# Performance work log

Measured on AMD Instinct MI355X. Metric: run time of the kernel, lower is better.

## Reference

```python
import jax, jax.numpy as jnp
import numpy as np

N, E, R = 50000, 300000, 4
F_IN, H, G, T = 11, 256, 2048, 19
BN_EPS = 1e-5


def _init_lin(key, fan_in, fan_out, extra=()):
    k1, k2 = jax.random.split(key)
    s = 1.0 / np.sqrt(fan_in)
    W = jax.random.uniform(k1, extra + (fan_in, fan_out), jnp.float32, -s, s)
    b = jax.random.uniform(k2, extra + (fan_out,), jnp.float32, -s, s)
    return W, b


def setup_inputs() -> dict:
    key = jax.random.key(0)
    ks = jax.random.split(key, 32)
    inp = {
        "x": jax.random.normal(ks[0], (N, F_IN), jnp.float32),
        "edge_index": jax.random.randint(ks[1], (2, E), 0, N, jnp.int64),
        "edge_type": jax.random.randint(ks[2], (E,), 0, R, jnp.int64),
        "batch": jnp.sort(jax.random.randint(ks[3], (N,), 0, G, jnp.int64)),
    }
    ki = 4
    for li, fin in ((1, F_IN), (2, H), (3, H)):
        sw, sb = _init_lin(ks[ki], fin, H); ki += 1
        w1, b1 = _init_lin(ks[ki], fin, H, (R,)); ki += 1
        w2, b2 = _init_lin(ks[ki], H, H, (R,)); ki += 1
        inp[f"l{li}_sw"], inp[f"l{li}_sb"] = sw, sb
        inp[f"l{li}_w1"], inp[f"l{li}_b1"] = w1, b1
        inp[f"l{li}_g"] = jnp.ones((R, H), jnp.float32)
        inp[f"l{li}_bt"] = jnp.zeros((R, H), jnp.float32)
        inp[f"l{li}_w2"], inp[f"l{li}_b2"] = w2, b2
    inp["lin_w"], inp["lin_b"] = _init_lin(ks[ki], H, T)
    return inp


def _rgin_layer(x, src, dst, rel_mask, sw, sb, w1, b1, g, bt, w2, b2):
    # self-loop linear
    out = x @ sw + sb
    msg = x[src]  # [E, d] gather of source features
    for i in range(R):
        # per-relation masked scatter-add aggregation at target nodes
        agg = jax.ops.segment_sum(msg * rel_mask[:, i:i + 1], dst, num_segments=N)
        h = x + agg  # GIN with eps=0: (1+eps)*x + sum_neighbors
        h = h @ w1[i] + b1[i]
        # BatchNorm1d (training-mode batch stats, biased var)
        mu = jnp.mean(h, axis=0)
        var = jnp.var(h, axis=0)
        h = (h - mu) * jax.lax.rsqrt(var + BN_EPS) * g[i] + bt[i]
        h = jax.nn.relu(h)
        out = out + h @ w2[i] + b2[i]
    return out


def reference(x, edge_index, edge_type, batch,
              l1_sw, l1_sb, l1_w1, l1_b1, l1_g, l1_bt, l1_w2, l1_b2,
              l2_sw, l2_sb, l2_w1, l2_b1, l2_g, l2_bt, l2_w2, l2_b2,
              l3_sw, l3_sb, l3_w1, l3_b1, l3_g, l3_bt, l3_w2, l3_b2,
              lin_w, lin_b):
    src, dst = edge_index[0], edge_index[1]
    rel_mask = jax.nn.one_hot(edge_type, R, dtype=x.dtype)  # [E, R]
    h = jax.nn.relu(_rgin_layer(x, src, dst, rel_mask, l1_sw, l1_sb, l1_w1, l1_b1, l1_g, l1_bt, l1_w2, l1_b2))
    h = jax.nn.relu(_rgin_layer(h, src, dst, rel_mask, l2_sw, l2_sb, l2_w1, l2_b1, l2_g, l2_bt, l2_w2, l2_b2))
    h = jax.nn.relu(_rgin_layer(h, src, dst, rel_mask, l3_sw, l3_sb, l3_w1, l3_b1, l3_g, l3_bt, l3_w2, l3_b2))
    # global mean pool over graphs
    pooled = jax.ops.segment_sum(h, batch, num_segments=G)
    counts = jax.ops.segment_sum(jnp.ones((N,), h.dtype), batch, num_segments=G)
    pooled = pooled / jnp.maximum(counts, 1.0)[:, None]
    return pooled @ lin_w + lin_b
```

## Files before the change

### kernel.cpp

```cpp
#include <hip/hip_runtime.h>

static const int kN = 50000;
static const int kE = 300000;
static const int kG = 2048;
static const int kT = 19;
static const int kSeg = kN * 4;
static const int kScanB = (kSeg + 256) / 256;

typedef __bf16 bf16;
typedef __bf16 bf16x8 __attribute__((ext_vector_type(8)));
typedef __bf16 bf16x4 __attribute__((ext_vector_type(4)));
typedef float  f32x4  __attribute__((ext_vector_type(4)));

__global__ __launch_bounds__(512) void k_rgin1(
    const bf16* __restrict__ Pb, const int* __restrict__ srcidx,
    const int* __restrict__ row_ptr, const bf16* __restrict__ w1t,
    bf16* __restrict__ h1, float* __restrict__ stats)
{
    __shared__ bf16 As[64][264];
    const int t = threadIdx.x;
    const int r = blockIdx.y;
    const int m0 = blockIdx.x * 64;
    const int wave = t >> 6, lane = t & 63;
    const int l15 = lane & 15, lq = lane >> 4, koff = lq * 8;
    const int wn = wave * 32;

    const bf16* Bt = w1t + (long)r * 65536;
    const bf16* Bp[2];
#pragma unroll
    for (int j = 0; j < 2; ++j)
        Bp[j] = Bt + (long)(wn + j * 16 + l15) * 256 + koff;
    bf16x8 b0[2], b1[2];
#pragma unroll
    for (int j = 0; j < 2; ++j) b0[j] = *(const bf16x8*)(Bp[j]);

    {
        const int rbase = m0 + wave * 8;
        int i0s[8], i1s[8];
#pragma unroll
        for (int rr = 0; rr < 8; ++rr) {
            int dc = rbase + rr; if (dc >= kN) dc = kN - 1;
            int seg = dc * 4 + r;
            i0s[rr] = row_ptr[seg];
            i1s[rr] = row_ptr[seg + 1];
        }
#pragma unroll
        for (int rr = 0; rr < 8; ++rr) {
            int dc = rbase + rr; if (dc >= kN) dc = kN - 1;
            bf16x4 sv = ((const bf16x4*)(Pb + (long)dc * 256))[lane];
            f32x4 a = {(float)sv[0], (float)sv[1], (float)sv[2], (float)sv[3]};
            int i = i0s[rr], i1 = i1s[rr];
            for (; i + 1 < i1; i += 2) {
                int s0 = srcidx[i], s1 = srcidx[i + 1];
                bf16x4 v0 = ((const bf16x4*)(Pb + (long)s0 * 256))[lane];
                bf16x4 v1 = ((const bf16x4*)(Pb + (long)s1 * 256))[lane];
                a[0] += (float)v0[0] + (float)v1[0];
                a[1] += (float)v0[1] + (float)v1[1];
                a[2] += (float)v0[2] + (float)v1[2];
                a[3] += (float)v0[3] + (float)v1[3];
            }
            if (i < i1) {
                bf16x4 v0 = ((const bf16x4*)(Pb + (long)srcidx[i] * 256))[lane];
                a[0] += (float)v0[0]; a[1] += (float)v0[1];
                a[2] += (float)v0[2]; a[3] += (float)v0[3];
            }
            bf16x4 o = {(bf16)a[0], (bf16)a[1], (bf16)a[2], (bf16)a[3]};
            *(bf16x4*)&As[wave * 8 + rr][lane * 4] = o;
        }
    }
    __syncthreads();

    const bf16* Ar[4];
#pragma unroll
    for (int i = 0; i < 4; ++i) Ar[i] = &As[i * 16 + l15][koff];

    f32x4 acc[4][2];
#pragma unroll
    for (int i = 0; i < 4; ++i)
#pragma unroll
        for (int j = 0; j < 2; ++j) acc[i][j] = (f32x4){0.f, 0.f, 0.f, 0.f};

#pragma unroll
    for (int kt = 0; kt < 256; kt += 32) {
        int kn = kt + 32; if (kn >= 256) kn = 0;
#pragma unroll
        for (int j = 0; j < 2; ++j) b1[j] = *(const bf16x8*)(Bp[j] + kn);
        bf16x8 a[4];
#pragma unroll
        for (int i = 0; i < 4; ++i) a[i] = *(const bf16x8*)(Ar[i] + kt);
#pragma unroll
        for (int i = 0; i < 4; ++i)
#pragma unroll
            for (int j = 0; j < 2; ++j)
                acc[i][j] = __builtin_amdgcn_mfma_f32_16x16x32_bf16(a[i], b0[j], acc[i][j], 0, 0, 0);
#pragma unroll
        for (int j = 0; j < 2; ++j) b0[j] = b1[j];
    }

    const int cB = r * 256;
    float sv[2] = {0, 0}, qv[2] = {0, 0};
#pragma unroll
    for (int i = 0; i < 4; ++i) {
        int rowb = m0 + i * 16 + lq * 4;
#pragma unroll
        for (int rr = 0; rr < 4; ++rr) {
            int gm = rowb + rr;
            if (gm < kN) {
#pragma unroll
                for (int j = 0; j < 2; ++j) {
                    int gn = wn + j * 16 + l15;
                    bf16 bv = (bf16)acc[i][j][rr];
                    h1[(long)gm * 1024 + cB + gn] = bv;
                    float f = (float)bv;
                    sv[j] += f; qv[j] += f * f;
                }
            }
        }
    }
#pragma unroll
    for (int j = 0; j < 2; ++j) {
        float s = sv[j], q = qv[j];
        s += __shfl_xor(s, 16); s += __shfl_xor(s, 32);
        q += __shfl_xor(q, 16); q += __shfl_xor(q, 32);
        if (lq == 0) {
            int gn = cB + wn + j * 16 + l15;
            atomicAdd(&stats[gn], s);
            atomicAdd(&stats[1024 + gn], q);
        }
    }
}

__global__ __launch_bounds__(512) void k_l1gemm(
    const bf16* __restrict__ a1b, const bf16* __restrict__ w1tL1,
    bf16* __restrict__ h1, float* __restrict__ stats)
{
    const int t = threadIdx.x;
    const int r = blockIdx.y;
    const int m0 = blockIdx.x * 128;
    const int wave = t >> 6, lane = t & 63;
    const int l15 = lane & 15, lq = lane >> 4, koff = lq * 8;
    const int wm = (wave & 1) * 64, wn = (wave >> 1) * 64;

    bf16x8 a[4], b[4];
#pragma unroll
    for (int i = 0; i < 4; ++i) {
        int gm = m0 + wm + i * 16 + l15;
        if (gm >= kN) gm = kN - 1;
        a[i] = *(const bf16x8*)(a1b + ((long)r * kN + gm) * 32 + koff);
    }
#pragma unroll
    for (int j = 0; j < 4; ++j)
        b[j] = *(const bf16x8*)(w1tL1 + (long)r * 8192 + (long)(wn + j * 16 + l15) * 32 + koff);

    f32x4 acc[4][4];
#pragma unroll
    for (int i = 0; i < 4; ++i)
#pragma unroll
        for (int j = 0; j < 4; ++j)
            acc[i][j] = __builtin_amdgcn_mfma_f32_16x16x32_bf16(a[i], b[j],
                        (f32x4){0.f, 0.f, 0.f, 0.f}, 0, 0, 0);

    const int cB = r * 256;
    float sv[4] = {0,0,0,0}, qv[4] = {0,0,0,0};
#pragma unroll
    for (int i = 0; i < 4; ++i) {
        int rowb = m0 + wm + i * 16 + lq * 4;
#pragma unroll
        for (int rr = 0; rr < 4; ++rr) {
            int gm = rowb + rr;
            if (gm < kN) {
#pragma unroll
                for (int j = 0; j < 4; ++j) {
                    int gn = wn + j * 16 + l15;
                    bf16 bv = (bf16)acc[i][j][rr];
                    h1[(long)gm * 1024 + cB + gn] = bv;
                    float f = (float)bv;
                    sv[j] += f; qv[j] += f * f;
                }
            }
        }
    }
#pragma unroll
    for (int j = 0; j < 4; ++j) {
        float s = sv[j], q = qv[j];
        s += __shfl_xor(s, 16); s += __shfl_xor(s, 32);
        q += __shfl_xor(q, 16); q += __shfl_xor(q, 32);
        if (lq == 0) {
            int gn = cB + wn + j * 16 + l15;
            atomicAdd(&stats[gn], s);
            atomicAdd(&stats[1024 + gn], q);
        }
    }
}

template<int CHUNKS, int C1, bool PoolOut>
__global__ __launch_bounds__(256) void k_gemm2(
    const bf16* __restrict__ A1, int lda1,
    const bf16* __restrict__ A2,
    const bf16* __restrict__ Bt,
    bf16* __restrict__ Cout,
    int M, const float* __restrict__ bias,
    const float* __restrict__ scl, const float* __restrict__ shf,
    const int* __restrict__ batch, float* __restrict__ pooled)
{
    constexpr int K = CHUNKS * 128;
    __shared__ bf16 As[2][64][136];
    const int t = threadIdx.x;
    const int wave = t >> 6, lane = t & 63;
    const int l15 = lane & 15, lq = lane >> 4, koff = lq * 8;
    const int wn = wave * 64;
    const int m0 = blockIdx.x * 64;

    const int srow = t >> 4;
    const int kg   = (t & 15) * 8;

    const bf16* Bp[4];
#pragma unroll
    for (int j = 0; j < 4; ++j)
        Bp[j] = Bt + (long)(wn + j * 16 + l15) * K + koff;

    f32x4 acc[4][4];
#pragma unroll
    for (int i = 0; i < 4; ++i)
#pragma unroll
        for (int j = 0; j < 4; ++j) acc[i][j] = (f32x4){0.f, 0.f, 0.f, 0.f};

    auto ld_raw = [&](int c, bf16x8* rv, float4* sf) {
#pragma unroll
        for (int i = 0; i < 4; ++i) {
            int gm = m0 + srow + i * 16; if (gm >= M) gm = M - 1;
            if (c < C1) rv[i] = *(const bf16x8*)(A1 + (long)gm * lda1 + c * 128 + kg);
            else        rv[i] = *(const bf16x8*)(A2 + (long)gm * 1024 + (c - C1) * 128 + kg);
        }
        if (c >= C1) {
            int k2 = (c - C1) * 128 + kg;
            sf[0] = *(const float4*)(scl + k2);
            sf[1] = *(const float4*)(scl + k2 + 4);
            sf[2] = *(const float4*)(shf + k2);
            sf[3] = *(const float4*)(shf + k2 + 4);
        }
    };
    auto st_lds = [&](int c, const bf16x8* rv, const float4* sf, int sel) {
        float sa[8], ta[8];
        if (c >= C1) {
            sa[0]=sf[0].x; sa[1]=sf[0].y; sa[2]=sf[0].z; sa[3]=sf[0].w;
            sa[4]=sf[1].x; sa[5]=sf[1].y; sa[6]=sf[1].z; sa[7]=sf[1].w;
            ta[0]=sf[2].x; ta[1]=sf[2].y; ta[2]=sf[2].z; ta[3]=sf[2].w;
            ta[4]=sf[3].x; ta[5]=sf[3].y; ta[6]=sf[3].z; ta[7]=sf[3].w;
        }
#pragma unroll
        for (int i = 0; i < 4; ++i) {
            bf16x8 v = rv[i];
            if (c >= C1) {
                bf16x8 o;
#pragma unroll
                for (int u = 0; u < 8; ++u)
                    o[u] = (bf16)fmaxf(0.f, fmaf((float)v[u], sa[u], ta[u]));
                v = o;
            }
            *(bf16x8*)&As[sel][srow + i * 16][kg] = v;
        }
    };

    bf16x8 rv[4]; float4 sf[4];
    ld_raw(0, rv, sf);
    bf16x8 breg[2][4];
#pragma unroll
    for (int j = 0; j < 4; ++j) breg[0][j] = *(const bf16x8*)(Bp[j]);
#pragma unroll
    for (int j = 0; j < 4; ++j) breg[1][j] = *(const bf16x8*)(Bp[j] + 32);
    st_lds(0, rv, sf, 0);
    __syncthreads();

    for (int c = 0; c < CHUNKS; ++c) {
        const int sel = c & 1;
        if (c + 1 < CHUNKS) ld_raw(c + 1, rv, sf);
#pragma unroll
        for (int ks = 0; ks < 4; ++ks) {
            bf16x8 a[4], bu[4];
#pragma unroll
            for (int i = 0; i < 4; ++i)
                a[i] = *(const bf16x8*)&As[sel][i * 16 + l15][ks * 32 + koff];
#pragma unroll
            for (int j = 0; j < 4; ++j) bu[j] = breg[ks & 1][j];
            int knext = (c * 4 + ks + 2) * 32; if (knext >= K) knext = 0;
#pragma unroll
            for (int j = 0; j < 4; ++j) breg[ks & 1][j] = *(const bf16x8*)(Bp[j] + knext);
#pragma unroll
            for (int i = 0; i < 4; ++i)
#pragma unroll
                for (int j = 0; j < 4; ++j)
                    acc[i][j] = __builtin_amdgcn_mfma_f32_16x16x32_bf16(a[i], bu[j], acc[i][j], 0, 0, 0);
        }
        if (c + 1 < CHUNKS) {
            st_lds(c + 1, rv, sf, sel ^ 1);
            __syncthreads();
        }
    }

#pragma unroll
    for (int i = 0; i < 4; ++i) {
        int rowb = m0 + i * 16 + lq * 4;
#pragma unroll
        for (int rr = 0; rr < 4; ++rr) {
            int gm = rowb + rr;
            if (gm < M) {
                int g = PoolOut ? batch[gm] : 0;
#pragma unroll
                for (int j = 0; j < 4; ++j) {
                    int gn = wn + j * 16 + l15;
                    float v = fmaxf(acc[i][j][rr] + bias[gn], 0.f);
                    if (PoolOut) atomicAdd(&pooled[(long)g * 256 + gn], v);
                    else         Cout[(long)gm * 256 + gn] = (bf16)v;
                }
            }
        }
    }
}

__global__ void k_hist(const int* __restrict__ ei, const int* __restrict__ et,
                       int* __restrict__ hist)
{
    int e = blockIdx.x * 256 + threadIdx.x;
    if (e >= kE) return;
    atomicAdd(&hist[ei[kE + e] * 4 + et[e]], 1);
}

__global__ void k_scan1(const int* __restrict__ hist, int* __restrict__ bsum)
{
    __shared__ int sd[256];
    int i = blockIdx.x * 256 + threadIdx.x;
    sd[threadIdx.x] = (i < kSeg) ? hist[i] : 0;
    __syncthreads();
    for (int o = 128; o > 0; o >>= 1) {
        if (threadIdx.x < o) sd[threadIdx.x] += sd[threadIdx.x + o];
        __syncthreads();
    }
    if (threadIdx.x == 0) bsum[blockIdx.x] = sd[0];
}

__global__ __launch_bounds__(1024) void k_scan2(const int* __restrict__ bsum,
                                                int* __restrict__ boff)
{
    __shared__ int sd[1024];
    int t = threadIdx.x;
    sd[t] = (t < kScanB) ? bsum[t] : 0;
    __syncthreads();
    for (int o = 1; o < 1024; o <<= 1) {
        int v = (t >= o) ? sd[t - o] : 0;
        __syncthreads();
        sd[t] += v;
        __syncthreads();
    }
    if (t < kScanB) boff[t] = (t == 0) ? 0 : sd[t - 1];
}

__global__ void k_scan3(const int* __restrict__ hist, const int* __restrict__ boff,
                        int* __restrict__ row_ptr, int* __restrict__ cursor)
{
    __shared__ int sd[256];
    int i = blockIdx.x * 256 + threadIdx.x;
    int v = (i < kSeg) ? hist[i] : 0;
    sd[threadIdx.x] = v;
    __syncthreads();
    for (int o = 1; o < 256; o <<= 1) {
        int u = (threadIdx.x >= o) ? sd[threadIdx.x - o] : 0;
        __syncthreads();
        sd[threadIdx.x] += u;
        __syncthreads();
    }
    if (i <= kSeg) {
        int excl = boff[blockIdx.x] + sd[threadIdx.x] - v;
        row_ptr[i] = excl;
        if (i < kSeg) cursor[i] = excl;
    }
}

__global__ void k_fill(const int* __restrict__ ei, const int* __restrict__ et,
                       int* __restrict__ cursor, int* __restrict__ srcidx)
{
    int e = blockIdx.x * 256 + threadIdx.x;
    if (e >= kE) return;
    int key = ei[kE + e] * 4 + et[e];
    int pos = atomicAdd(&cursor[key], 1);
    srcidx[pos] = ei[e];
}

__global__ void k_agg11(const float* __restrict__ x, const int* __restrict__ srcidx,
                        const int* __restrict__ row_ptr, bf16* __restrict__ a1b)
{
    long gid = (long)blockIdx.x * 256 + threadIdx.x;
    if (gid >= (long)kSeg * 32) return;
    int ch  = (int)(gid & 31);
    int seg = (int)(gid >> 5);
    int d = seg >> 2, r = seg & 3;
    float acc = 0.f;
    if (ch < 11) {
        acc = x[(long)d * 11 + ch];
        int i0 = row_ptr[seg], i1 = row_ptr[seg + 1];
        for (int i = i0; i < i1; ++i) acc += x[(long)srcidx[i] * 11 + ch];
    }
    a1b[((long)r * kN + d) * 32 + ch] = (bf16)acc;
}

__global__ void k_xpad(const float* __restrict__ x, bf16* __restrict__ xb1)
{
    long gid = (long)blockIdx.x * 256 + threadIdx.x;
    if (gid >= (long)kN * 128) return;
    int c = (int)(gid & 127); long d = gid >> 7;
    xb1[gid] = (c < 11) ? (bf16)x[d * 11 + c] : (bf16)0.f;
}

__global__ void k_wt_s(const float* __restrict__ in, bf16* __restrict__ out,
                       int K, int N, int ldout, int coff)
{
    int i = blockIdx.x * 256 + threadIdx.x;
    if (i >= K * N) return;
    int n = i / K, k = i - n * K;
    out[(long)n * ldout + coff + k] = (bf16)in[(long)k * N + n];
}

__global__ void k_wtL1(const float* __restrict__ w1, bf16* __restrict__ out)
{
    int i = blockIdx.x * 256 + threadIdx.x;
    if (i >= 4 * 256 * 32) return;
    int r = i >> 13, rem = i & 8191, n = rem >> 5, k = rem & 31;
    out[i] = (k < 11) ? (bf16)w1[(long)r * 11 * 256 + (long)k * 256 + n] : (bf16)0.f;
}

__global__ void k_bn_params(const float* __restrict__ stats,
                            const float* __restrict__ g, const float* __restrict__ bt,
                            float* __restrict__ scl, float* __restrict__ shf)
{
    int c = blockIdx.x * 256 + threadIdx.x;
    const float invN = 1.0f / (float)kN;
    float mu  = stats[c] * invN;
    float var = stats[1024 + c] * invN - mu * mu;
    float sc  = g[c] * rsqrtf(var + 1e-5f);
    scl[c] = sc;
    shf[c] = bt[c] - mu * sc;
}

__global__ void k_bias_total(const float* sb0, const float* b20,
                             const float* sb1, const float* b21,
                             const float* sb2, const float* b22,
                             float* __restrict__ btt)
{
    int l = blockIdx.x, j = threadIdx.x;
    const float* sb = (l == 0) ? sb0 : (l == 1) ? sb1 : sb2;
    const float* b2 = (l == 0) ? b20 : (l == 1) ? b21 : b22;
    float v = sb[j];
#pragma unroll
    for (int r = 0; r < 4; ++r) v += b2[r * 256 + j];
    btt[l * 256 + j] = v;
}

__global__ void k_counts(const int* __restrict__ batch, float* __restrict__ counts)
{
    int v = blockIdx.x * 256 + threadIdx.x;
    if (v < kN) atomicAdd(&counts[batch[v]], 1.0f);
}

__global__ __launch_bounds__(64) void k_head(const float* __restrict__ pooled,
                                             const float* __restrict__ counts,
                                             const float* __restrict__ lw,
                                             const float* __restrict__ lb,
                                             float* __restrict__ out)
{
    int g = blockIdx.x;
    int l = threadIdx.x;
    float inv = 1.0f / fmaxf(counts[g], 1.0f);
    float acc[kT];
#pragma unroll
    for (int t = 0; t < kT; ++t) acc[t] = 0.f;
    for (int k = l; k < 256; k += 64) {
        float p = pooled[((long)g << 8) + k] * inv;
#pragma unroll
        for (int t = 0; t < kT; ++t) acc[t] = fmaf(p, lw[k * kT + t], acc[t]);
    }
#pragma unroll
    for (int off = 32; off > 0; off >>= 1)
#pragma unroll
        for (int t = 0; t < kT; ++t) acc[t] += __shfl_down(acc[t], off);
    if (l == 0) {
#pragma unroll
        for (int t = 0; t < kT; ++t) out[(long)g * kT + t] = acc[t] + lb[t];
    }
}

extern "C" void kernel_launch(void* const* d_in, const int* in_sizes, int n_in,
                              void* d_out, int out_size, void* d_ws, size_t ws_size,
                              hipStream_t stream)
{
    const float* x     = (const float*)d_in[0];
    const int*   ei    = (const int*)d_in[1];
    const int*   et    = (const int*)d_in[2];
    const int*   batch = (const int*)d_in[3];

    const float *sw[3], *sb[3], *w1[3], *gmm[3], *btm[3], *w2[3], *b2[3];
    for (int l = 0; l < 3; ++l) {
        int b = 4 + l * 8;
        sw[l]  = (const float*)d_in[b + 0];
        sb[l]  = (const float*)d_in[b + 1];
        w1[l]  = (const float*)d_in[b + 2];
        gmm[l] = (const float*)d_in[b + 4];
        btm[l] = (const float*)d_in[b + 5];
        w2[l]  = (const float*)d_in[b + 6];
        b2[l]  = (const float*)d_in[b + 7];
    }
    const float* lin_w = (const float*)d_in[28];
    const float* lin_b = (const float*)d_in[29];
    float* out = (float*)d_out;
    (void)in_sizes; (void)n_in; (void)out_size;

    char* wsb = (char*)d_ws;
    size_t off = 0;
    auto alloc = [&](size_t bytes) { void* p = wsb + off; off = (off + bytes + 255) & ~(size_t)255; return p; };
    bf16*  Pb0    = (bf16*) alloc((size_t)kN * 256 * 2);
    bf16*  Pb1    = (bf16*) alloc((size_t)kN * 256 * 2);
    bf16*  h1     = (bf16*) alloc((size_t)kN * 1024 * 2);
    bf16*  a1b    = (bf16*) alloc((size_t)4 * kN * 32 * 2);
    bf16*  xb1    = (bf16*) alloc((size_t)kN * 128 * 2);
    bf16*  w1t    = (bf16*) alloc((size_t)2 * 4 * 65536 * 2);
    bf16*  w1tL1  = (bf16*) alloc((size_t)4 * 256 * 32 * 2);
    bf16*  Bc0    = (bf16*) alloc((size_t)256 * 1152 * 2);
    bf16*  Bc1    = (bf16*) alloc((size_t)256 * 1280 * 2);
    bf16*  Bc2    = (bf16*) alloc((size_t)256 * 1280 * 2);
    int*   hist   = (int*)  alloc((size_t)(kSeg + 1) * 4);
    int*   row_ptr= (int*)  alloc((size_t)(kSeg + 1) * 4);
    int*   cursor = (int*)  alloc((size_t)kSeg * 4);
    int*   srcidx = (int*)  alloc((size_t)kE * 4);
    int*   bsum   = (int*)  alloc((size_t)kScanB * 4);
    int*   boff   = (int*)  alloc((size_t)kScanB * 4);
    float* stats  = (float*)alloc(2048 * 4);
    float* scl    = (float*)alloc(1024 * 4);
    float* shf    = (float*)alloc(1024 * 4);
    float* btt    = (float*)alloc(3 * 256 * 4);
    float* pooled = (float*)alloc((size_t)kG * 256 * 4);
    float* counts = (float*)alloc(kG * 4);
    if (ws_size < off) return;

    const dim3 gL1((kN + 127) / 128, 4);
    const dim3 gR((kN + 63) / 64, 4);
    const dim3 g2((kN + 63) / 64);

    hipMemsetAsync(hist, 0, (size_t)(kSeg + 1) * 4, stream);
    k_hist<<<(kE + 255) / 256, 256, 0, stream>>>(ei, et, hist);
    k_scan1<<<kScanB, 256, 0, stream>>>(hist, bsum);
    k_scan2<<<1, 1024, 0, stream>>>(bsum, boff);
    k_scan3<<<kScanB, 256, 0, stream>>>(hist, boff, row_ptr, cursor);
    k_fill<<<(kE + 255) / 256, 256, 0, stream>>>(ei, et, cursor, srcidx);

    k_bias_total<<<3, 256, 0, stream>>>(sb[0], b2[0], sb[1], b2[1], sb[2], b2[2], btt);
    k_xpad<<<(int)(((long)kN * 128 + 255) / 256), 256, 0, stream>>>(x, xb1);
    k_wtL1<<<(4 * 256 * 32 + 255) / 256, 256, 0, stream>>>(w1[0], w1tL1);
    for (int l = 1; l < 3; ++l)
        for (int r = 0; r < 4; ++r)
            k_wt_s<<<256, 256, 0, stream>>>(w1[l] + (long)r * 65536,
                                            w1t + (long)(l - 1) * 4 * 65536 + (long)r * 65536,
                                            256, 256, 256, 0);
    hipMemsetAsync(Bc0, 0, (size_t)256 * 1152 * 2, stream);
    k_wt_s<<<(11 * 256 + 255) / 256, 256, 0, stream>>>(sw[0], Bc0, 11, 256, 1152, 0);
    k_wt_s<<<1024, 256, 0, stream>>>(w2[0], Bc0, 1024, 256, 1152, 128);
    k_wt_s<<<256, 256, 0, stream>>>(sw[1], Bc1, 256, 256, 1280, 0);
    k_wt_s<<<1024, 256, 0, stream>>>(w2[1], Bc1, 1024, 256, 1280, 256);
    k_wt_s<<<256, 256, 0, stream>>>(sw[2], Bc2, 256, 256, 1280, 0);
    k_wt_s<<<1024, 256, 0, stream>>>(w2[2], Bc2, 1024, 256, 1280, 256);

    k_counts<<<(kN + 255) / 256, 256, 0, stream>>>(batch, counts);
    hipMemsetAsync(pooled, 0, (size_t)kG * 256 * 4, stream);

    k_agg11<<<(int)(((long)kSeg * 32 + 255) / 256), 256, 0, stream>>>(x, srcidx, row_ptr, a1b);
    hipMemsetAsync(stats, 0, 2048 * 4, stream);
    k_l1gemm<<<gL1, 512, 0, stream>>>(a1b, w1tL1, h1, stats);
    k_bn_params<<<4, 256, 0, stream>>>(stats, gmm[0], btm[0], scl, shf);
    k_gemm2<9, 1, false><<<g2, 256, 0, stream>>>(xb1, 128, h1, Bc0,
                                                 Pb0, kN, btt + 0, scl, shf, nullptr, nullptr);

    hipMemsetAsync(stats, 0, 2048 * 4, stream);
    k_rgin1<<<gR, 512, 0, stream>>>(Pb0, srcidx, row_ptr, w1t, h1, stats);
    k_bn_params<<<4, 256, 0, stream>>>(stats, gmm[1], btm[1], scl, shf);
    k_gemm2<10, 2, false><<<g2, 256, 0, stream>>>(Pb0, 256, h1, Bc1,
                                                  Pb1, kN, btt + 256, scl, shf, nullptr, nullptr);

    hipMemsetAsync(stats, 0, 2048 * 4, stream);
    k_rgin1<<<gR, 512, 0, stream>>>(Pb1, srcidx, row_ptr, w1t + (size_t)4 * 65536, h1, stats);
    k_bn_params<<<4, 256, 0, stream>>>(stats, gmm[2], btm[2], scl, shf);
    k_gemm2<10, 2, true><<<g2, 256, 0, stream>>>(Pb1, 256, h1, Bc2,
                                                 nullptr, kN, btt + 512, scl, shf, batch, pooled);

    k_head<<<kG, 64, 0, stream>>>(pooled, counts, lin_w, lin_b, out);
}
```

Baseline: 1.004 ms.

## Restructure gemm2 to 512 threads with 2x4 wave tiling and 256-wide K chunks

The second-stage GEMM moves from 4 waves (each owning a 64x64 tile) to 8 waves arranged 2x4 (each owning a 32x64 tile). K is staged in 256-wide chunks with a single LDS buffer instead of double-buffered 128-wide chunks. Layer 1 is padded to K=1280 so all three layers share one code path, at the cost of a larger padded self-loop input and extra zero MACs. The aim is more waves per block to hide latency, but each B fragment now feeds only 2 MFMAs instead of 4, and the single buffer needs two barriers per chunk.

```diff
diff --git a/kernel.cpp b/kernel.cpp
--- a/kernel.cpp
+++ b/kernel.cpp
@@ -193,9 +193,9 @@
     }
 }
 
-template<int CHUNKS, int C1, bool PoolOut>
-__global__ __launch_bounds__(256) void k_gemm2(
-    const bf16* __restrict__ A1, int lda1,
+template<bool PoolOut>
+__global__ __launch_bounds__(512) void k_gemm2(
+    const bf16* __restrict__ A1,
     const bf16* __restrict__ A2,
     const bf16* __restrict__ Bt,
     bf16* __restrict__ Cout,
@@ -203,62 +203,63 @@
     const float* __restrict__ scl, const float* __restrict__ shf,
     const int* __restrict__ batch, float* __restrict__ pooled)
 {
-    constexpr int K = CHUNKS * 128;
-    __shared__ bf16 As[2][64][136];
+    constexpr int K = 1280;
+    __shared__ bf16 As[64][264];
     const int t = threadIdx.x;
     const int wave = t >> 6, lane = t & 63;
     const int l15 = lane & 15, lq = lane >> 4, koff = lq * 8;
-    const int wn = wave * 64;
+    const int wm = (wave & 1) * 32;
+    const int wn = (wave >> 1) * 64;
     const int m0 = blockIdx.x * 64;
 
-    const int srow = t >> 4;
-    const int kg   = (t & 15) * 8;
+    const int srow = t >> 5;
+    const int c8   = (t & 31) * 8;
 
     const bf16* Bp[4];
 #pragma unroll
     for (int j = 0; j < 4; ++j)
         Bp[j] = Bt + (long)(wn + j * 16 + l15) * K + koff;
 
-    f32x4 acc[4][4];
-#pragma unroll
-    for (int i = 0; i < 4; ++i)
+    f32x4 acc[2][4];
+#pragma unroll
+    for (int i = 0; i < 2; ++i)
 #pragma unroll
         for (int j = 0; j < 4; ++j) acc[i][j] = (f32x4){0.f, 0.f, 0.f, 0.f};
 
     auto ld_raw = [&](int c, bf16x8* rv, float4* sf) {
 #pragma unroll
-        for (int i = 0; i < 4; ++i) {
-            int gm = m0 + srow + i * 16; if (gm >= M) gm = M - 1;
-            if (c < C1) rv[i] = *(const bf16x8*)(A1 + (long)gm * lda1 + c * 128 + kg);
-            else        rv[i] = *(const bf16x8*)(A2 + (long)gm * 1024 + (c - C1) * 128 + kg);
-        }
-        if (c >= C1) {
-            int k2 = (c - C1) * 128 + kg;
+        for (int u = 0; u < 4; ++u) {
+            int gm = m0 + srow + u * 16; if (gm >= M) gm = M - 1;
+            if (c == 0) rv[u] = *(const bf16x8*)(A1 + (long)gm * 256 + c8);
+            else        rv[u] = *(const bf16x8*)(A2 + (long)gm * 1024 + (c - 1) * 256 + c8);
+        }
+        if (c > 0) {
+            int k2 = (c - 1) * 256 + c8;
             sf[0] = *(const float4*)(scl + k2);
             sf[1] = *(const float4*)(scl + k2 + 4);
             sf[2] = *(const float4*)(shf + k2);
             sf[3] = *(const float4*)(shf + k2 + 4);
         }
     };
-    auto st_lds = [&](int c, const bf16x8* rv, const float4* sf, int sel) {
+    auto st_lds = [&](int c, const bf16x8* rv, const float4* sf) {
         float sa[8], ta[8];
-        if (c >= C1) {
+        if (c > 0) {
             sa[0]=sf[0].x; sa[1]=sf[0].y; sa[2]=sf[0].z; sa[3]=sf[0].w;
             sa[4]=sf[1].x; sa[5]=sf[1].y; sa[6]=sf[1].z; sa[7]=sf[1].w;
             ta[0]=sf[2].x; ta[1]=sf[2].y; ta[2]=sf[2].z; ta[3]=sf[2].w;
             ta[4]=sf[3].x; ta[5]=sf[3].y; ta[6]=sf[3].z; ta[7]=sf[3].w;
         }
 #pragma unroll
-        for (int i = 0; i < 4; ++i) {
-            bf16x8 v = rv[i];
-            if (c >= C1) {
+        for (int u = 0; u < 4; ++u) {
+            bf16x8 v = rv[u];
+            if (c > 0) {
                 bf16x8 o;
 #pragma unroll
-                for (int u = 0; u < 8; ++u)
-                    o[u] = (bf16)fmaxf(0.f, fmaf((float)v[u], sa[u], ta[u]));
+                for (int w = 0; w < 8; ++w)
+                    o[w] = (bf16)fmaxf(0.f, fmaf((float)v[w], sa[w], ta[w]));
                 v = o;
             }
-            *(bf16x8*)&As[sel][srow + i * 16][kg] = v;
+            *(bf16x8*)&As[srow + u * 16][c8] = v;
         }
     };
 
@@ -269,38 +270,38 @@
     for (int j = 0; j < 4; ++j) breg[0][j] = *(const bf16x8*)(Bp[j]);
 #pragma unroll
     for (int j = 0; j < 4; ++j) breg[1][j] = *(const bf16x8*)(Bp[j] + 32);
-    st_lds(0, rv, sf, 0);
+    st_lds(0, rv, sf);
     __syncthreads();
 
-    for (int c = 0; c < CHUNKS; ++c) {
-        const int sel = c & 1;
-        if (c + 1 < CHUNKS) ld_raw(c + 1, rv, sf);
-#pragma unroll
-        for (int ks = 0; ks < 4; ++ks) {
-            bf16x8 a[4], bu[4];
-#pragma unroll
-            for (int i = 0; i < 4; ++i)
-                a[i] = *(const bf16x8*)&As[sel][i * 16 + l15][ks * 32 + koff];
+    for (int c = 0; c < 5; ++c) {
+        if (c + 1 < 5) ld_raw(c + 1, rv, sf);
+#pragma unroll
+        for (int ks = 0; ks < 8; ++ks) {
+            bf16x8 a[2], bu[4];
+#pragma unroll
+            for (int i = 0; i < 2; ++i)
+                a[i] = *(const bf16x8*)&As[wm + i * 16 + l15][ks * 32 + koff];
 #pragma unroll
             for (int j = 0; j < 4; ++j) bu[j] = breg[ks & 1][j];
-            int knext = (c * 4 + ks + 2) * 32; if (knext >= K) knext = 0;
+            int knext = c * 256 + (ks + 2) * 32; if (knext >= K) knext = 0;
 #pragma unroll
             for (int j = 0; j < 4; ++j) breg[ks & 1][j] = *(const bf16x8*)(Bp[j] + knext);
 #pragma unroll
-            for (int i = 0; i < 4; ++i)
+            for (int i = 0; i < 2; ++i)
 #pragma unroll
                 for (int j = 0; j < 4; ++j)
                     acc[i][j] = __builtin_amdgcn_mfma_f32_16x16x32_bf16(a[i], bu[j], acc[i][j], 0, 0, 0);
         }
-        if (c + 1 < CHUNKS) {
-            st_lds(c + 1, rv, sf, sel ^ 1);
+        if (c + 1 < 5) {
             __syncthreads();
-        }
-    }
-
-#pragma unroll
-    for (int i = 0; i < 4; ++i) {
-        int rowb = m0 + i * 16 + lq * 4;
+            st_lds(c + 1, rv, sf);
+            __syncthreads();
+        }
+    }
+
+#pragma unroll
+    for (int i = 0; i < 2; ++i) {
+        int rowb = m0 + wm + i * 16 + lq * 4;
 #pragma unroll
         for (int rr = 0; rr < 4; ++rr) {
             int gm = rowb + rr;
@@ -406,8 +407,8 @@
 __global__ void k_xpad(const float* __restrict__ x, bf16* __restrict__ xb1)
 {
     long gid = (long)blockIdx.x * 256 + threadIdx.x;
-    if (gid >= (long)kN * 128) return;
-    int c = (int)(gid & 127); long d = gid >> 7;
+    if (gid >= (long)kN * 256) return;
+    int c = (int)(gid & 255); long d = gid >> 8;
     xb1[gid] = (c < 11) ? (bf16)x[d * 11 + c] : (bf16)0.f;
 }
 
@@ -520,10 +521,10 @@
     bf16*  Pb1    = (bf16*) alloc((size_t)kN * 256 * 2);
     bf16*  h1     = (bf16*) alloc((size_t)kN * 1024 * 2);
     bf16*  a1b    = (bf16*) alloc((size_t)4 * kN * 32 * 2);
-    bf16*  xb1    = (bf16*) alloc((size_t)kN * 128 * 2);
+    bf16*  xb1    = (bf16*) alloc((size_t)kN * 256 * 2);
     bf16*  w1t    = (bf16*) alloc((size_t)2 * 4 * 65536 * 2);
     bf16*  w1tL1  = (bf16*) alloc((size_t)4 * 256 * 32 * 2);
-    bf16*  Bc0    = (bf16*) alloc((size_t)256 * 1152 * 2);
+    bf16*  Bc0    = (bf16*) alloc((size_t)256 * 1280 * 2);
     bf16*  Bc1    = (bf16*) alloc((size_t)256 * 1280 * 2);
     bf16*  Bc2    = (bf16*) alloc((size_t)256 * 1280 * 2);
     int*   hist   = (int*)  alloc((size_t)(kSeg + 1) * 4);
@@ -552,16 +553,16 @@
     k_fill<<<(kE + 255) / 256, 256, 0, stream>>>(ei, et, cursor, srcidx);
 
     k_bias_total<<<3, 256, 0, stream>>>(sb[0], b2[0], sb[1], b2[1], sb[2], b2[2], btt);
-    k_xpad<<<(int)(((long)kN * 128 + 255) / 256), 256, 0, stream>>>(x, xb1);
+    k_xpad<<<(int)(((long)kN * 256 + 255) / 256), 256, 0, stream>>>(x, xb1);
     k_wtL1<<<(4 * 256 * 32 + 255) / 256, 256, 0, stream>>>(w1[0], w1tL1);
     for (int l = 1; l < 3; ++l)
         for (int r = 0; r < 4; ++r)
             k_wt_s<<<256, 256, 0, stream>>>(w1[l] + (long)r * 65536,
                                             w1t + (long)(l - 1) * 4 * 65536 + (long)r * 65536,
                                             256, 256, 256, 0);
-    hipMemsetAsync(Bc0, 0, (size_t)256 * 1152 * 2, stream);
-    k_wt_s<<<(11 * 256 + 255) / 256, 256, 0, stream>>>(sw[0], Bc0, 11, 256, 1152, 0);
-    k_wt_s<<<1024, 256, 0, stream>>>(w2[0], Bc0, 1024, 256, 1152, 128);
+    hipMemsetAsync(Bc0, 0, (size_t)256 * 1280 * 2, stream);
+    k_wt_s<<<(11 * 256 + 255) / 256, 256, 0, stream>>>(sw[0], Bc0, 11, 256, 1280, 0);
+    k_wt_s<<<1024, 256, 0, stream>>>(w2[0], Bc0, 1024, 256, 1280, 256);
     k_wt_s<<<256, 256, 0, stream>>>(sw[1], Bc1, 256, 256, 1280, 0);
     k_wt_s<<<1024, 256, 0, stream>>>(w2[1], Bc1, 1024, 256, 1280, 256);
     k_wt_s<<<256, 256, 0, stream>>>(sw[2], Bc2, 256, 256, 1280, 0);
@@ -574,20 +575,20 @@
     hipMemsetAsync(stats, 0, 2048 * 4, stream);
     k_l1gemm<<<gL1, 512, 0, stream>>>(a1b, w1tL1, h1, stats);
     k_bn_params<<<4, 256, 0, stream>>>(stats, gmm[0], btm[0], scl, shf);
-    k_gemm2<9, 1, false><<<g2, 256, 0, stream>>>(xb1, 128, h1, Bc0,
-                                                 Pb0, kN, btt + 0, scl, shf, nullptr, nullptr);
+    k_gemm2<false><<<g2, 512, 0, stream>>>(xb1, h1, Bc0,
+                                           Pb0, kN, btt + 0, scl, shf, nullptr, nullptr);
 
     hipMemsetAsync(stats, 0, 2048 * 4, stream);
     k_rgin1<<<gR, 512, 0, stream>>>(Pb0, srcidx, row_ptr, w1t, h1, stats);
     k_bn_params<<<4, 256, 0, stream>>>(stats, gmm[1], btm[1], scl, shf);
-    k_gemm2<10, 2, false><<<g2, 256, 0, stream>>>(Pb0, 256, h1, Bc1,
-                                                  Pb1, kN, btt + 256, scl, shf, nullptr, nullptr);
+    k_gemm2<false><<<g2, 512, 0, stream>>>(Pb0, h1, Bc1,
+                                           Pb1, kN, btt + 256, scl, shf, nullptr, nullptr);
 
     hipMemsetAsync(stats, 0, 2048 * 4, stream);
     k_rgin1<<<gR, 512, 0, stream>>>(Pb1, srcidx, row_ptr, w1t + (size_t)4 * 65536, h1, stats);
     k_bn_params<<<4, 256, 0, stream>>>(stats, gmm[2], btm[2], scl, shf);
-    k_gemm2<10, 2, true><<<g2, 256, 0, stream>>>(Pb1, 256, h1, Bc2,
-                                                 nullptr, kN, btt + 512, scl, shf, batch, pooled);
+    k_gemm2<true><<<g2, 512, 0, stream>>>(Pb1, h1, Bc2,
+                                          nullptr, kN, btt + 512, scl, shf, batch, pooled);
 
     k_head<<<kG, 64, 0, stream>>>(pooled, counts, lin_w, lin_b, out);
 }
```

After: 1.236 ms. 1.23x slower.
